# Kernel tuning notes

Measured on AMD Instinct MI355X. Metric: run time of the kernel, lower is better.

The kernel has to match this reference:

```python
import jax, jax.numpy as jnp
import numpy as np

H = 512   # embedding_dim (forced by Attention(512,512))
F = 21    # n_features
T = 28    # output_length

def _cell(x, h, c, Wih, Whh, b):
    # PyTorch LSTMCell math, gate order i,f,g,o
    g = x @ Wih.T + h @ Whh.T + b
    i, f, gg, o = jnp.split(g, 4, axis=-1)
    c2 = jax.nn.sigmoid(f) * c + jax.nn.sigmoid(i) * jnp.tanh(gg)
    h2 = jax.nn.sigmoid(o) * jnp.tanh(c2)
    return h2, c2

def _lstm3(inp, h, c, Wih0, Wih1, Wih2, Whh, bih, bhh):
    # 3-layer LSTM, single time step. h,c: [3,1,H]
    Wihs = (Wih0, Wih1, Wih2)
    hs, cs = [], []
    x = inp
    for l in range(3):
        hl, cl = _cell(x, h[l], c[l], Wihs[l], Whh[l], bih[l] + bhh[l])
        hs.append(hl); cs.append(cl)
        x = hl
    return x, jnp.stack(hs), jnp.stack(cs)

def setup_inputs() -> dict:
    key = jax.random.key(0)
    ks = jax.random.split(key, 20)
    s = 0.05
    f32 = jnp.float32
    return {
        "x": jax.random.normal(ks[0], (1, F), f32),
        "prev_y": jax.random.normal(ks[1], (1, F), f32),
        "enc_Wih0": jax.random.normal(ks[2], (4*H, F), f32) * s,
        "enc_Wih1": jax.random.normal(ks[3], (4*H, H), f32) * s,
        "enc_Wih2": jax.random.normal(ks[4], (4*H, H), f32) * s,
        "enc_Whh": jax.random.normal(ks[5], (3, 4*H, H), f32) * s,
        "enc_bih": jax.random.normal(ks[6], (3, 4*H), f32) * s,
        "enc_bhh": jax.random.normal(ks[7], (3, 4*H), f32) * s,
        "attn_W": jax.random.normal(ks[8], (H, 2*H), f32) * s,
        "attn_b": jax.random.normal(ks[9], (H,), f32) * s,
        "v_W": jax.random.normal(ks[10], (1, H), f32) * s,
        "dec_Wih0": jax.random.normal(ks[11], (4*H, H+F), f32) * s,
        "dec_Wih1": jax.random.normal(ks[12], (4*H, H), f32) * s,
        "dec_Wih2": jax.random.normal(ks[13], (4*H, H), f32) * s,
        "dec_Whh": jax.random.normal(ks[14], (3, 4*H, H), f32) * s,
        "dec_bih": jax.random.normal(ks[15], (3, 4*H), f32) * s,
        "dec_bhh": jax.random.normal(ks[16], (3, 4*H), f32) * s,
        "out_W": jax.random.normal(ks[17], (F, 2*H), f32) * s,
        "out_b": jax.random.normal(ks[18], (F,), f32) * s,
    }

def reference(x, prev_y, enc_Wih0, enc_Wih1, enc_Wih2, enc_Whh, enc_bih, enc_bhh,
              attn_W, attn_b, v_W, dec_Wih0, dec_Wih1, dec_Wih2, dec_Whh, dec_bih, dec_bhh,
              out_W, out_b):
    z = jnp.zeros((3, 1, H), x.dtype)
    # Encoder: single time step over feature-as-sequence input [1, F]
    enc_out, h, c = _lstm3(x, z, z, enc_Wih0, enc_Wih1, enc_Wih2, enc_Whh, enc_bih, enc_bhh)
    # enc_out: [1, H]; src_len == 1

    def step(carry, _):
        prev_out, h, c = carry
        # Bahdanau attention (src_len = 1)
        cat = jnp.concatenate([h[2], enc_out], axis=-1)          # [1, 2H]
        energy = jnp.tanh(cat @ attn_W.T + attn_b)               # [1, H]
        score = energy @ v_W.T                                    # [1, 1]
        a = jax.nn.softmax(score, axis=1)                         # [1, 1] (== 1)
        weighted = a * enc_out                                    # [1, H]
        rnn_in = jnp.concatenate([prev_out, weighted], axis=-1)  # [1, H+F]
        out, h2, c2 = _lstm3(rnn_in, h, c, dec_Wih0, dec_Wih1, dec_Wih2, dec_Whh, dec_bih, dec_bhh)
        y = jnp.concatenate([out, weighted], axis=-1) @ out_W.T + out_b  # [1, F]
        return (y, h2, c2), y

    _, ys = jax.lax.scan(step, (prev_y, h, c), None, length=T)
    return ys  # [T, 1, F]
```

## Files before the change

### kernel.cpp

```cpp
#include <hip/hip_runtime.h>
#include <cstddef>

constexpr int H  = 512;
constexpr int F  = 21;
constexpr int T  = 28;
constexpr int PB = 128;
constexpr int NB = PB + 1;
constexpr int NT = 256;
constexpr int NW = NT / 64;

#define SCOPE_AGENT __HIP_MEMORY_SCOPE_AGENT

__device__ unsigned long long g_hp[2][3][H];
__device__ unsigned long long g_hy[T][H];
__device__ unsigned g_epoch;

struct P {
  const float *x, *py, *eW0, *eW1, *eW2, *ebih, *ebhh;
  const float *dW0, *dW1, *dW2, *dWhh, *dbih, *dbhh, *outW, *outb;
  float* out;
};

__device__ __forceinline__ float sigm(float v)  { return 1.0f / (1.0f + __expf(-v)); }
__device__ __forceinline__ float tanh_f(float v){ return 1.0f - 2.0f / (__expf(2.0f * v) + 1.0f); }

__device__ __forceinline__ float4 wredsum4(float4 v) {
#pragma unroll
  for (int off = 32; off > 0; off >>= 1) {
    v.x += __shfl_xor(v.x, off, 64);
    v.y += __shfl_xor(v.y, off, 64);
    v.z += __shfl_xor(v.z, off, 64);
    v.w += __shfl_xor(v.w, off, 64);
  }
  return v;
}
__device__ __forceinline__ float wredsum1(float v) {
#pragma unroll
  for (int off = 32; off > 0; off >>= 1) v += __shfl_xor(v, off, 64);
  return v;
}

__device__ __forceinline__ void pput(unsigned long long* slot, float v, unsigned tag) {
  union { float f; unsigned u; } c; c.f = v;
  unsigned long long pk = ((unsigned long long)tag << 32) | (unsigned long long)c.u;
  (void)__hip_atomic_exchange(slot, pk, __ATOMIC_RELAXED, SCOPE_AGENT);
}
__device__ __forceinline__ unsigned long long tld(const unsigned long long* q) {
  return __hip_atomic_load(q, __ATOMIC_RELAXED, SCOPE_AGENT);
}
__device__ __forceinline__ float fbits(unsigned long long v) {
  union { unsigned u; float f; } c; c.u = (unsigned)v; return c.f;
}

__device__ __forceinline__ void stagev(const unsigned long long* __restrict__ A,
                                       unsigned wa, float* __restrict__ dst) {
  const int i = threadIdx.x;
  unsigned long long v0 = tld(A + i), v1 = tld(A + i + NT);
  int guard = 0;
  while ((((unsigned)(v0 >> 32)) != wa || ((unsigned)(v1 >> 32)) != wa) &&
         ++guard < (1 << 20)) {
    v0 = tld(A + i); v1 = tld(A + i + NT);
  }
  dst[i] = fbits(v0); dst[i + NT] = fbits(v1);
  __syncthreads();
}

struct W8 { float4 a[4]; float4 b[4]; };

__device__ __forceinline__ W8 ldw_g(const float* __restrict__ W, int r, int lane) {
  W8 o;
#pragma unroll
  for (int g = 0; g < 4; ++g) {
    const float* q = W + (size_t)(g * H + r) * H + lane * 8;
    o.a[g] = *(const float4*)q;
    o.b[g] = *(const float4*)(q + 4);
  }
  return o;
}
__device__ __forceinline__ W8 ldw_lds(const float* sM, int w, int lane) {
  W8 o;
#pragma unroll
  for (int g = 0; g < 4; ++g) {
    const float* q = sM + (w * 4 + g) * H + lane * 8;
    o.a[g] = *(const float4*)q;
    o.b[g] = *(const float4*)(q + 4);
  }
  return o;
}
__device__ __forceinline__ void fma8(const W8& wt, const float4& x0, const float4& x1,
                                     float s[4]) {
#pragma unroll
  for (int g = 0; g < 4; ++g) {
    s[g] += wt.a[g].x * x0.x + wt.a[g].y * x0.y + wt.a[g].z * x0.z + wt.a[g].w * x0.w
          + wt.b[g].x * x1.x + wt.b[g].y * x1.y + wt.b[g].z * x1.z + wt.b[g].w * x1.w;
  }
}

__device__ __forceinline__ float cellup(const float4& v, const float b[4], float& c) {
  float cn = sigm(v.y + b[1]) * c + sigm(v.x + b[0]) * tanh_f(v.z + b[2]);
  c = cn;
  return sigm(v.w + b[3]) * tanh_f(cn);
}

__device__ __forceinline__ void write_y_frag(const P& p, int trow, int w, int lane,
                                             const float4& h0, const float4& h1,
                                             const float* sYe) {
  for (int j = w; j < F; j += NW) {
    const float* q = p.outW + (size_t)j * (2 * H) + lane * 8;
    float4 w0 = *(const float4*)q;
    float4 w1 = *(const float4*)(q + 4);
    float s = w0.x * h0.x + w0.y * h0.y + w0.z * h0.z + w0.w * h0.w
            + w1.x * h1.x + w1.y * h1.y + w1.z * h1.z + w1.w * h1.w;
    s = wredsum1(s);
    if (lane == 0) p.out[trow * F + j] = s + sYe[j];
  }
}

__global__ __launch_bounds__(NT, 1)
void k_flow(P p) {
  const int lane = threadIdx.x & 63;
  const int w    = threadIdx.x >> 6;
  const unsigned tg =
      __hip_atomic_load(&g_epoch, __ATOMIC_RELAXED, SCOPE_AGENT) << 6;

  __shared__ float sM[NW * 4 * H];
  __shared__ float sBuf[2][H];
  __shared__ float senc[H];
  __shared__ float sYe[F + 3];

  if (blockIdx.x == PB) {
    stagev(g_hp[1][2], tg + 1u, senc);
    {
      float4 e0 = *(const float4*)(senc + lane * 8);
      float4 e1 = *(const float4*)(senc + lane * 8 + 4);
      for (int j = w; j < F; j += NW) {
        const float* q = p.outW + (size_t)j * (2 * H) + H + lane * 8;
        float4 w0 = *(const float4*)q;
        float4 w1 = *(const float4*)(q + 4);
        float s = w0.x * e0.x + w0.y * e0.y + w0.z * e0.z + w0.w * e0.w
                + w1.x * e1.x + w1.y * e1.y + w1.z * e1.z + w1.w * e1.w;
        s = wredsum1(s);
        if (lane == 0) sYe[j] = s + p.outb[j];
      }
      __syncthreads();
    }
    for (int t = 0; t < T; ++t) {
      float* xb = sBuf[t & 1];
      stagev(g_hy[t], tg + (unsigned)(t + 2), xb);
      float4 h20 = *(const float4*)(xb + lane * 8);
      float4 h21 = *(const float4*)(xb + lane * 8 + 4);
      write_y_frag(p, t, w, lane, h20, h21, sYe);
    }
    if (threadIdx.x == 0)
      __hip_atomic_fetch_add(&g_epoch, 1u, __ATOMIC_RELAXED, SCOPE_AGENT);
  } else {
    const int r = blockIdx.x * NW + w;

    float c0 = 0.f, c1 = 0.f, c2 = 0.f;
    float b00[4], b0p[4], b1s[4], b2s[4];
    float sOld0[4] = {0, 0, 0, 0}, sOld1[4] = {0, 0, 0, 0}, sOld2[4] = {0, 0, 0, 0};
    int bi = 0;

    {
      float s0 = 0.f, s1 = 0.f, s2 = 0.f, s3 = 0.f;
      if (lane < F) {
        const float xv = p.x[lane];
        s0 = p.eW0[(size_t)(0 * H + r) * F + lane] * xv;
        s1 = p.eW0[(size_t)(1 * H + r) * F + lane] * xv;
        s2 = p.eW0[(size_t)(2 * H + r) * F + lane] * xv;
        s3 = p.eW0[(size_t)(3 * H + r) * F + lane] * xv;
      }
      float4 v = wredsum4(make_float4(s0, s1, s2, s3));
      if (lane == 0) {
        const float* bi_ = p.ebih + r;
        const float* bh_ = p.ebhh + r;
        float cn = sigm(v.x + bi_[0] + bh_[0]) * tanh_f(v.z + bi_[2 * H] + bh_[2 * H]);
        c0 = cn;
        pput(&g_hp[1][0][r], sigm(v.w + bi_[3 * H] + bh_[3 * H]) * tanh_f(cn), tg + 1u);
      }
    }

    {
      float4 mA[4], mB[4];
#pragma unroll
      for (int g = 0; g < 4; ++g) {
        mA[g] = make_float4(0.f, 0.f, 0.f, 0.f);
        mB[g] = make_float4(0.f, 0.f, 0.f, 0.f);
      }
      for (int f = 0; f < F; ++f) {
        const float* q = p.outW + (size_t)f * (2 * H) + lane * 8;
        const float4 oa = *(const float4*)q;
        const float4 ob = *(const float4*)(q + 4);
#pragma unroll
        for (int g = 0; g < 4; ++g) {
          const float wf = p.dW0[(size_t)(g * H + r) * (H + F) + f];
          mA[g].x += wf * oa.x; mA[g].y += wf * oa.y; mA[g].z += wf * oa.z; mA[g].w += wf * oa.w;
          mB[g].x += wf * ob.x; mB[g].y += wf * ob.y; mB[g].z += wf * ob.z; mB[g].w += wf * ob.w;
        }
      }
#pragma unroll
      for (int g = 0; g < 4; ++g) {
        *(float4*)(sM + (w * 4 + g) * H + lane * 8)     = mA[g];
        *(float4*)(sM + (w * 4 + g) * H + lane * 8 + 4) = mB[g];
      }
    }
#pragma unroll
    for (int g = 0; g < 4; ++g) {
      b1s[g] = p.dbih[4 * H + g * H + r] + p.dbhh[4 * H + g * H + r];
      b2s[g] = p.dbih[8 * H + g * H + r] + p.dbhh[8 * H + g * H + r];
    }

    {
      W8 wt = ldw_g(p.eW1, r, lane);
      stagev(g_hp[1][0], tg + 1u, sBuf[0]);
      float4 a0 = *(const float4*)(sBuf[0] + lane * 8);
      float4 a1 = *(const float4*)(sBuf[0] + lane * 8 + 4);
      float s[4] = {0.f, 0.f, 0.f, 0.f};
      fma8(wt, a0, a1, s);
      float4 v = wredsum4(make_float4(s[0], s[1], s[2], s[3]));
      if (lane == 0) {
        const float* bi_ = p.ebih + 4 * H + r;
        const float* bh_ = p.ebhh + 4 * H + r;
        float cn = sigm(v.x + bi_[0] + bh_[0]) * tanh_f(v.z + bi_[2 * H] + bh_[2 * H]);
        c1 = cn;
        pput(&g_hp[1][1][r], sigm(v.w + bi_[3 * H] + bh_[3 * H]) * tanh_f(cn), tg + 1u);
      }
    }

    {
      W8 wt  = ldw_g(p.eW2, r, lane);
      W8 wh1 = ldw_g(p.dWhh + (size_t)4 * H * H, r, lane);
      stagev(g_hp[1][1], tg + 1u, sBuf[1]);
      float4 a0 = *(const float4*)(sBuf[1] + lane * 8);
      float4 a1 = *(const float4*)(sBuf[1] + lane * 8 + 4);
      float s[4] = {0.f, 0.f, 0.f, 0.f};
      fma8(wt, a0, a1, s);
      float4 v = wredsum4(make_float4(s[0], s[1], s[2], s[3]));
      if (lane == 0) {
        const float* bi_ = p.ebih + 8 * H + r;
        const float* bh_ = p.ebhh + 8 * H + r;
        float cn = sigm(v.x + bi_[0] + bh_[0]) * tanh_f(v.z + bi_[2 * H] + bh_[2 * H]);
        c2 = cn;
        pput(&g_hp[1][2][r], sigm(v.w + bi_[3 * H] + bh_[3 * H]) * tanh_f(cn), tg + 1u);
      }
      fma8(wh1, a0, a1, sOld1);
    }

    {
      W8 wh2 = ldw_g(p.dWhh + (size_t)8 * H * H, r, lane);
      stagev(g_hp[1][2], tg + 1u, senc);
      float4 e0 = *(const float4*)(senc + lane * 8);
      float4 e1 = *(const float4*)(senc + lane * 8 + 4);
      for (int j = w; j < F; j += NW) {
        const float* q = p.outW + (size_t)j * (2 * H) + H + lane * 8;
        float4 w0 = *(const float4*)q;
        float4 w1 = *(const float4*)(q + 4);
        float s = w0.x * e0.x + w0.y * e0.y + w0.z * e0.z + w0.w * e0.w
                + w1.x * e1.x + w1.y * e1.y + w1.z * e1.z + w1.w * e1.w;
        s = wredsum1(s);
        if (lane == 0) sYe[j] = s + p.outb[j];
      }
      {
        float sg[4];
#pragma unroll
        for (int g = 0; g < 4; ++g) {
          const float* q = p.dW0 + (size_t)(g * H + r) * (H + F) + F + lane * 8;
          sg[g] = q[0] * e0.x + q[1] * e0.y + q[2] * e0.z + q[3] * e0.w
                + q[4] * e1.x + q[5] * e1.y + q[6] * e1.z + q[7] * e1.w;
        }
        float4 v = wredsum4(make_float4(sg[0], sg[1], sg[2], sg[3]));
        if (lane == 0) {
          b0p[0] = v.x + p.dbih[0 * H + r] + p.dbhh[0 * H + r];
          b0p[1] = v.y + p.dbih[1 * H + r] + p.dbhh[1 * H + r];
          b0p[2] = v.z + p.dbih[2 * H + r] + p.dbhh[2 * H + r];
          b0p[3] = v.w + p.dbih[3 * H + r] + p.dbhh[3 * H + r];
        }
      }
      {
        float f0 = 0.f, f1 = 0.f, f2 = 0.f, f3 = 0.f;
        if (lane < F) {
          const float yv = p.py[lane];
          f0 = p.dW0[(size_t)(0 * H + r) * (H + F) + lane] * yv;
          f1 = p.dW0[(size_t)(1 * H + r) * (H + F) + lane] * yv;
          f2 = p.dW0[(size_t)(2 * H + r) * (H + F) + lane] * yv;
          f3 = p.dW0[(size_t)(3 * H + r) * (H + F) + lane] * yv;
        }
        float4 v = wredsum4(make_float4(f0, f1, f2, f3));
        if (lane == 0) {
          b00[0] = b0p[0] + v.x; b00[1] = b0p[1] + v.y;
          b00[2] = b0p[2] + v.z; b00[3] = b0p[3] + v.w;
        }
      }
      __syncthreads();
      {
        float f0 = 0.f, f1 = 0.f, f2 = 0.f, f3 = 0.f;
        if (lane < F) {
          const float yv = sYe[lane];
          f0 = p.dW0[(size_t)(0 * H + r) * (H + F) + lane] * yv;
          f1 = p.dW0[(size_t)(1 * H + r) * (H + F) + lane] * yv;
          f2 = p.dW0[(size_t)(2 * H + r) * (H + F) + lane] * yv;
          f3 = p.dW0[(size_t)(3 * H + r) * (H + F) + lane] * yv;
        }
        float4 v = wredsum4(make_float4(f0, f1, f2, f3));
        if (lane == 0) {
          b0p[0] += v.x; b0p[1] += v.y; b0p[2] += v.z; b0p[3] += v.w;
        }
      }
      fma8(wh2, e0, e1, sOld2);
    }

    {
      W8 wh0 = ldw_g(p.dWhh, r, lane);
      float4 a0 = *(const float4*)(sBuf[0] + lane * 8);
      float4 a1 = *(const float4*)(sBuf[0] + lane * 8 + 4);
      float s[4] = {0.f, 0.f, 0.f, 0.f};
      fma8(wh0, a0, a1, s);
      float4 v = wredsum4(make_float4(s[0], s[1], s[2], s[3]));
      if (lane == 0) pput(&g_hp[0][0][r], cellup(v, b00, c0), tg + 2u);
    }
    __syncthreads();

    for (int t = 0; t < T; ++t) {
      const int pb = t & 1, ob = pb ^ 1;
      const unsigned wn = tg + (unsigned)(t + 2);
      const unsigned wo = wn - 1u;

      if (t >= 1) {
        W8 wh2 = ldw_g(p.dWhh + (size_t)8 * H * H, r, lane);
        stagev(g_hp[ob][2], wo, sBuf[bi]);
        W8 wm = ldw_lds(sM, w, lane);
        float4 h20 = *(const float4*)(sBuf[bi] + lane * 8);
        float4 h21 = *(const float4*)(sBuf[bi] + lane * 8 + 4);
        float s[4] = {sOld0[0], sOld0[1], sOld0[2], sOld0[3]};
        fma8(wm, h20, h21, s);
        float4 v = wredsum4(make_float4(s[0], s[1], s[2], s[3]));
        if (lane == 0) pput(&g_hp[pb][0][r], cellup(v, b0p, c0), wn);
        sOld2[0] = sOld2[1] = sOld2[2] = sOld2[3] = 0.f;
        fma8(wh2, h20, h21, sOld2);
        bi ^= 1;
      }

      {
        W8 wi  = ldw_g(p.dW1, r, lane);
        W8 wh0 = ldw_g(p.dWhh, r, lane);
        stagev(g_hp[pb][0], wn, sBuf[bi]);
        float4 a0 = *(const float4*)(sBuf[bi] + lane * 8);
        float4 a1 = *(const float4*)(sBuf[bi] + lane * 8 + 4);
        float s[4] = {sOld1[0], sOld1[1], sOld1[2], sOld1[3]};
        fma8(wi, a0, a1, s);
        float4 v = wredsum4(make_float4(s[0], s[1], s[2], s[3]));
        if (lane == 0) pput(&g_hp[pb][1][r], cellup(v, b1s, c1), wn);
        sOld0[0] = sOld0[1] = sOld0[2] = sOld0[3] = 0.f;
        fma8(wh0, a0, a1, sOld0);
        bi ^= 1;
      }
      {
        W8 wi  = ldw_g(p.dW2, r, lane);
        W8 wh1 = ldw_g(p.dWhh + (size_t)4 * H * H, r, lane);
        stagev(g_hp[pb][1], wn, sBuf[bi]);
        float4 a0 = *(const float4*)(sBuf[bi] + lane * 8);
        float4 a1 = *(const float4*)(sBuf[bi] + lane * 8 + 4);
        float s[4] = {sOld2[0], sOld2[1], sOld2[2], sOld2[3]};
        fma8(wi, a0, a1, s);
        float4 v = wredsum4(make_float4(s[0], s[1], s[2], s[3]));
        if (lane == 0) {
          float hv = cellup(v, b2s, c2);
          pput(&g_hp[pb][2][r], hv, wn);
          pput(&g_hy[t][r], hv, wn);
        }
        sOld1[0] = sOld1[1] = sOld1[2] = sOld1[3] = 0.f;
        fma8(wh1, a0, a1, sOld1);
        bi ^= 1;
      }
    }
  }
}

extern "C" void kernel_launch(void* const* d_in, const int* in_sizes, int n_in,
                              void* d_out, int out_size, void* d_ws, size_t ws_size,
                              hipStream_t stream) {
  P p;
  p.x    = (const float*)d_in[0];
  p.py   = (const float*)d_in[1];
  p.eW0  = (const float*)d_in[2];
  p.eW1  = (const float*)d_in[3];
  p.eW2  = (const float*)d_in[4];
  p.ebih = (const float*)d_in[6];
  p.ebhh = (const float*)d_in[7];
  p.dW0  = (const float*)d_in[11];
  p.dW1  = (const float*)d_in[12];
  p.dW2  = (const float*)d_in[13];
  p.dWhh = (const float*)d_in[14];
  p.dbih = (const float*)d_in[15];
  p.dbhh = (const float*)d_in[16];
  p.outW = (const float*)d_in[17];
  p.outb = (const float*)d_in[18];
  p.out  = (float*)d_out;

  hipLaunchKernelGGL(k_flow, dim3(NB), dim3(NT), 0, stream, p);
}
```

Before: 318.8 us.

## Replace tagged 64-bit handoff slots with zero-sentinel float slots replicated across shards

The exchange of hidden states between blocks no longer packs a 32-bit epoch tag with each float in 64-bit atomics. Every recurrent phase gets its own float slot, and readers poll until the value is nonzero, reading two floats per 64-bit load. Each writer stores its value into four replicated copies so that polling blocks spread across different memory lines. Blocks zero the other parity buffer on exit so it is ready for the next launch. The change halves the data polled and spreads polling contention, but a state that is exactly 0.0 would cause a read to spin until the guard expires, and it relies on the zeroing holding across launches.

```diff
diff --git a/kernel.cpp b/kernel.cpp
--- a/kernel.cpp
+++ b/kernel.cpp
@@ -8,12 +8,17 @@
 constexpr int NB = PB + 1;
 constexpr int NT = 256;
 constexpr int NW = NT / 64;
+constexpr int KR = 4;
+constexpr int PH = 3 + 3 * T;
 
 #define SCOPE_AGENT __HIP_MEMORY_SCOPE_AGENT
 
-__device__ unsigned long long g_hp[2][3][H];
-__device__ unsigned long long g_hy[T][H];
+__device__ float g_hs[KR][2][PH][H];
 __device__ unsigned g_epoch;
+
+__device__ __forceinline__ int phS0(int t) { return 3 + 3 * t; }
+__device__ __forceinline__ int phS1(int t) { return 4 + 3 * t; }
+__device__ __forceinline__ int phS2(int t) { return 5 + 3 * t; }
 
 struct P {
   const float *x, *py, *eW0, *eW1, *eW2, *ebih, *ebhh;
@@ -40,28 +45,24 @@
   return v;
 }
 
-__device__ __forceinline__ void pput(unsigned long long* slot, float v, unsigned tag) {
-  union { float f; unsigned u; } c; c.f = v;
-  unsigned long long pk = ((unsigned long long)tag << 32) | (unsigned long long)c.u;
-  (void)__hip_atomic_exchange(slot, pk, __ATOMIC_RELAXED, SCOPE_AGENT);
-}
-__device__ __forceinline__ unsigned long long tld(const unsigned long long* q) {
-  return __hip_atomic_load(q, __ATOMIC_RELAXED, SCOPE_AGENT);
-}
-__device__ __forceinline__ float fbits(unsigned long long v) {
-  union { unsigned u; float f; } c; c.u = (unsigned)v; return c.f;
-}
-
-__device__ __forceinline__ void stagev(const unsigned long long* __restrict__ A,
-                                       unsigned wa, float* __restrict__ dst) {
+__device__ __forceinline__ void pput4(int par, int ph, int r, float v) {
+#pragma unroll
+  for (int k = 0; k < KR; ++k)
+    __hip_atomic_store(&g_hs[k][par][ph][r], v, __ATOMIC_RELAXED, SCOPE_AGENT);
+}
+
+__device__ __forceinline__ void stagev(const float* __restrict__ A,
+                                       float* __restrict__ dst) {
   const int i = threadIdx.x;
-  unsigned long long v0 = tld(A + i), v1 = tld(A + i + NT);
+  const unsigned long long* q = (const unsigned long long*)A + i;
+  unsigned long long v = __hip_atomic_load(q, __ATOMIC_RELAXED, SCOPE_AGENT);
   int guard = 0;
-  while ((((unsigned)(v0 >> 32)) != wa || ((unsigned)(v1 >> 32)) != wa) &&
+  while (((unsigned)v == 0u || (unsigned)(v >> 32) == 0u) &&
          ++guard < (1 << 20)) {
-    v0 = tld(A + i); v1 = tld(A + i + NT);
-  }
-  dst[i] = fbits(v0); dst[i + NT] = fbits(v1);
+    v = __hip_atomic_load(q, __ATOMIC_RELAXED, SCOPE_AGENT);
+  }
+  *(float2*)(dst + 2 * i) =
+      make_float2(__uint_as_float((unsigned)v), __uint_as_float((unsigned)(v >> 32)));
   __syncthreads();
 }
 
@@ -120,8 +121,10 @@
 void k_flow(P p) {
   const int lane = threadIdx.x & 63;
   const int w    = threadIdx.x >> 6;
-  const unsigned tg =
-      __hip_atomic_load(&g_epoch, __ATOMIC_RELAXED, SCOPE_AGENT) << 6;
+  const int sh   = blockIdx.x & (KR - 1);
+  const unsigned ep =
+      __hip_atomic_load(&g_epoch, __ATOMIC_RELAXED, SCOPE_AGENT);
+  const int par = (int)(ep & 1u);
 
   __shared__ float sM[NW * 4 * H];
   __shared__ float sBuf[2][H];
@@ -129,7 +132,7 @@
   __shared__ float sYe[F + 3];
 
   if (blockIdx.x == PB) {
-    stagev(g_hp[1][2], tg + 1u, senc);
+    stagev(g_hs[sh][par][2], senc);
     {
       float4 e0 = *(const float4*)(senc + lane * 8);
       float4 e1 = *(const float4*)(senc + lane * 8 + 4);
@@ -146,7 +149,7 @@
     }
     for (int t = 0; t < T; ++t) {
       float* xb = sBuf[t & 1];
-      stagev(g_hy[t], tg + (unsigned)(t + 2), xb);
+      stagev(g_hs[sh][par][phS2(t)], xb);
       float4 h20 = *(const float4*)(xb + lane * 8);
       float4 h21 = *(const float4*)(xb + lane * 8 + 4);
       write_y_frag(p, t, w, lane, h20, h21, sYe);
@@ -176,7 +179,7 @@
         const float* bh_ = p.ebhh + r;
         float cn = sigm(v.x + bi_[0] + bh_[0]) * tanh_f(v.z + bi_[2 * H] + bh_[2 * H]);
         c0 = cn;
-        pput(&g_hp[1][0][r], sigm(v.w + bi_[3 * H] + bh_[3 * H]) * tanh_f(cn), tg + 1u);
+        pput4(par, 0, r, sigm(v.w + bi_[3 * H] + bh_[3 * H]) * tanh_f(cn));
       }
     }
 
@@ -212,7 +215,7 @@
 
     {
       W8 wt = ldw_g(p.eW1, r, lane);
-      stagev(g_hp[1][0], tg + 1u, sBuf[0]);
+      stagev(g_hs[sh][par][0], sBuf[0]);
       float4 a0 = *(const float4*)(sBuf[0] + lane * 8);
       float4 a1 = *(const float4*)(sBuf[0] + lane * 8 + 4);
       float s[4] = {0.f, 0.f, 0.f, 0.f};
@@ -223,14 +226,14 @@
         const float* bh_ = p.ebhh + 4 * H + r;
         float cn = sigm(v.x + bi_[0] + bh_[0]) * tanh_f(v.z + bi_[2 * H] + bh_[2 * H]);
         c1 = cn;
-        pput(&g_hp[1][1][r], sigm(v.w + bi_[3 * H] + bh_[3 * H]) * tanh_f(cn), tg + 1u);
+        pput4(par, 1, r, sigm(v.w + bi_[3 * H] + bh_[3 * H]) * tanh_f(cn));
       }
     }
 
     {
       W8 wt  = ldw_g(p.eW2, r, lane);
       W8 wh1 = ldw_g(p.dWhh + (size_t)4 * H * H, r, lane);
-      stagev(g_hp[1][1], tg + 1u, sBuf[1]);
+      stagev(g_hs[sh][par][1], sBuf[1]);
       float4 a0 = *(const float4*)(sBuf[1] + lane * 8);
       float4 a1 = *(const float4*)(sBuf[1] + lane * 8 + 4);
       float s[4] = {0.f, 0.f, 0.f, 0.f};
@@ -241,14 +244,14 @@
         const float* bh_ = p.ebhh + 8 * H + r;
         float cn = sigm(v.x + bi_[0] + bh_[0]) * tanh_f(v.z + bi_[2 * H] + bh_[2 * H]);
         c2 = cn;
-        pput(&g_hp[1][2][r], sigm(v.w + bi_[3 * H] + bh_[3 * H]) * tanh_f(cn), tg + 1u);
+        pput4(par, 2, r, sigm(v.w + bi_[3 * H] + bh_[3 * H]) * tanh_f(cn));
       }
       fma8(wh1, a0, a1, sOld1);
     }
 
     {
       W8 wh2 = ldw_g(p.dWhh + (size_t)8 * H * H, r, lane);
-      stagev(g_hp[1][2], tg + 1u, senc);
+      stagev(g_hs[sh][par][2], senc);
       float4 e0 = *(const float4*)(senc + lane * 8);
       float4 e1 = *(const float4*)(senc + lane * 8 + 4);
       for (int j = w; j < F; j += NW) {
@@ -316,25 +319,21 @@
       float s[4] = {0.f, 0.f, 0.f, 0.f};
       fma8(wh0, a0, a1, s);
       float4 v = wredsum4(make_float4(s[0], s[1], s[2], s[3]));
-      if (lane == 0) pput(&g_hp[0][0][r], cellup(v, b00, c0), tg + 2u);
+      if (lane == 0) pput4(par, phS0(0), r, cellup(v, b00, c0));
     }
     __syncthreads();
 
     for (int t = 0; t < T; ++t) {
-      const int pb = t & 1, ob = pb ^ 1;
-      const unsigned wn = tg + (unsigned)(t + 2);
-      const unsigned wo = wn - 1u;
-
       if (t >= 1) {
         W8 wh2 = ldw_g(p.dWhh + (size_t)8 * H * H, r, lane);
-        stagev(g_hp[ob][2], wo, sBuf[bi]);
+        stagev(g_hs[sh][par][phS2(t - 1)], sBuf[bi]);
         W8 wm = ldw_lds(sM, w, lane);
         float4 h20 = *(const float4*)(sBuf[bi] + lane * 8);
         float4 h21 = *(const float4*)(sBuf[bi] + lane * 8 + 4);
         float s[4] = {sOld0[0], sOld0[1], sOld0[2], sOld0[3]};
         fma8(wm, h20, h21, s);
         float4 v = wredsum4(make_float4(s[0], s[1], s[2], s[3]));
-        if (lane == 0) pput(&g_hp[pb][0][r], cellup(v, b0p, c0), wn);
+        if (lane == 0) pput4(par, phS0(t), r, cellup(v, b0p, c0));
         sOld2[0] = sOld2[1] = sOld2[2] = sOld2[3] = 0.f;
         fma8(wh2, h20, h21, sOld2);
         bi ^= 1;
@@ -343,13 +342,13 @@
       {
         W8 wi  = ldw_g(p.dW1, r, lane);
         W8 wh0 = ldw_g(p.dWhh, r, lane);
-        stagev(g_hp[pb][0], wn, sBuf[bi]);
+        stagev(g_hs[sh][par][phS0(t)], sBuf[bi]);
         float4 a0 = *(const float4*)(sBuf[bi] + lane * 8);
         float4 a1 = *(const float4*)(sBuf[bi] + lane * 8 + 4);
         float s[4] = {sOld1[0], sOld1[1], sOld1[2], sOld1[3]};
         fma8(wi, a0, a1, s);
         float4 v = wredsum4(make_float4(s[0], s[1], s[2], s[3]));
-        if (lane == 0) pput(&g_hp[pb][1][r], cellup(v, b1s, c1), wn);
+        if (lane == 0) pput4(par, phS1(t), r, cellup(v, b1s, c1));
         sOld0[0] = sOld0[1] = sOld0[2] = sOld0[3] = 0.f;
         fma8(wh0, a0, a1, sOld0);
         bi ^= 1;
@@ -357,21 +356,24 @@
       {
         W8 wi  = ldw_g(p.dW2, r, lane);
         W8 wh1 = ldw_g(p.dWhh + (size_t)4 * H * H, r, lane);
-        stagev(g_hp[pb][1], wn, sBuf[bi]);
+        stagev(g_hs[sh][par][phS1(t)], sBuf[bi]);
         float4 a0 = *(const float4*)(sBuf[bi] + lane * 8);
         float4 a1 = *(const float4*)(sBuf[bi] + lane * 8 + 4);
         float s[4] = {sOld2[0], sOld2[1], sOld2[2], sOld2[3]};
         fma8(wi, a0, a1, s);
         float4 v = wredsum4(make_float4(s[0], s[1], s[2], s[3]));
-        if (lane == 0) {
-          float hv = cellup(v, b2s, c2);
-          pput(&g_hp[pb][2][r], hv, wn);
-          pput(&g_hy[t][r], hv, wn);
-        }
+        if (lane == 0) pput4(par, phS2(t), r, cellup(v, b2s, c2));
         sOld1[0] = sOld1[1] = sOld1[2] = sOld1[3] = 0.f;
         fma8(wh1, a0, a1, sOld1);
         bi ^= 1;
       }
+    }
+
+    {
+      const int r0 = blockIdx.x * NW;
+      const float4 z4 = make_float4(0.f, 0.f, 0.f, 0.f);
+      for (int idx = threadIdx.x; idx < KR * PH; idx += NT)
+        *(float4*)&g_hs[idx / PH][par ^ 1][idx % PH][r0] = z4;
     }
   }
 }
```

Result: faster. 306.7 us (median of 2 runs) (-3.8%).
